# Optimization experiments

Hardware: AMD Instinct MI355X
Metric: run time of the kernel (lower is better)

The kernel has to match this reference:

```python
import jax, jax.numpy as jnp
import numpy as np

D = 512
K = 32
B = 2
L = 2048


def setup_inputs() -> dict:
    key = jax.random.key(0)
    ks = jax.random.split(key, 12)
    s = 1.0 / np.sqrt(D)
    return {
        "x": jax.random.normal(ks[0], (B, L, D), dtype=jnp.float32),
        "W1": jax.random.normal(ks[1], (D, D), dtype=jnp.float32) * s,
        "b1": jnp.zeros((D,), jnp.float32),
        "W2": jax.random.normal(ks[2], (D, K), dtype=jnp.float32) * s,
        "b2": jnp.zeros((K,), jnp.float32),
        "pos_scale": jnp.array([0.5], jnp.float32),
        "content_scale": jnp.array([0.5], jnp.float32),
        "Wv": jax.random.normal(ks[3], (D, D), dtype=jnp.float32) * s,
        "bv": jnp.zeros((D,), jnp.float32),
        "ln_g": jnp.ones((D,), jnp.float32),
        "ln_b": jnp.zeros((D,), jnp.float32),
        "Wo": jax.random.normal(ks[4], (D, D), dtype=jnp.float32) * s,
        "bo": jnp.zeros((D,), jnp.float32),
    }


def reference(x, W1, b1, W2, b2, pos_scale, content_scale, Wv, bv, ln_g, ln_b, Wo, bo):
    Bb, Ll, Dd = x.shape
    Kk = W2.shape[1]
    # fixed positional phases: outer(positions, 1/10000^(k/K))
    freqs = 1.0 / (10000.0 ** (jnp.arange(Kk, dtype=jnp.float32) / Kk))
    pos_phase = jnp.arange(Ll, dtype=jnp.float32)[:, None] * freqs[None, :]  # [L,K]
    # content phase: Linear -> Tanh -> Linear, then tanh * pi
    h = jnp.tanh(x @ W1 + b1)
    content_phase = jnp.tanh(h @ W2 + b2) * jnp.pi  # [B,L,K]
    total_phase = pos_scale * pos_phase[None] + content_scale * content_phase  # [B,L,K]
    value = x @ Wv + bv  # [B,L,D]
    c = jnp.cos(total_phase)
    s = jnp.sin(total_phase)
    # phasor outer-product bind: [B,L,K,D]
    bound_real = c[..., None] * value[:, :, None, :]
    bound_imag = s[..., None] * value[:, :, None, :]
    mem_real = jnp.cumsum(bound_real, axis=1)
    mem_imag = jnp.cumsum(bound_imag, axis=1)
    retrieved = (mem_real * c[..., None] + mem_imag * s[..., None]).sum(axis=2)  # [B,L,D]
    norm = jnp.sqrt(jnp.arange(1, Ll + 1, dtype=jnp.float32) * Kk)[None, :, None]
    retrieved = retrieved / norm
    # to_out: LayerNorm then Linear
    mu = retrieved.mean(axis=-1, keepdims=True)
    var = retrieved.var(axis=-1, keepdims=True)
    ln = (retrieved - mu) / jnp.sqrt(var + 1e-5) * ln_g + ln_b
    return x + ln @ Wo + bo
```

## Files before the change

### kernel.cpp

```cpp
#include <hip/hip_runtime.h>
#include <hip/hip_bf16.h>
#include <math.h>

#define BB   2
#define LL   2048
#define DD   512
#define KK   32
#define BL   (BB*LL)
#define NCH  64

typedef unsigned short ushort_t;
typedef __bf16 bf16x8 __attribute__((ext_vector_type(8)));
typedef float  f32x4  __attribute__((ext_vector_type(4)));
typedef unsigned short ushort8 __attribute__((ext_vector_type(8)));

__device__ __forceinline__ void gl_lds16(const void* g, void* l) {
    __builtin_amdgcn_global_load_lds(
        (const __attribute__((address_space(1))) void*)g,
        (__attribute__((address_space(3))) void*)l, 16, 0, 0);
}
__device__ __forceinline__ ushort_t f2b(float f) {
    __bf16 b = (__bf16)f; return *(ushort_t*)&b;
}
__device__ __forceinline__ float b2f(ushort_t u) {
    unsigned int x = ((unsigned int)u) << 16; return *(float*)&x;
}

__global__ __launch_bounds__(256) void prep(const float* __restrict__ W1,
                                            const float* __restrict__ Wv,
                                            const float* __restrict__ Wo,
                                            const float* __restrict__ W2,
                                            const float* __restrict__ x,
                                            const float* __restrict__ lng,
                                            const float* __restrict__ lnb,
                                            const float* __restrict__ bo,
                                            __hip_bfloat16* __restrict__ Wct,
                                            __hip_bfloat16* __restrict__ Wot,
                                            __hip_bfloat16* __restrict__ W2T,
                                            __hip_bfloat16* __restrict__ xb,
                                            float* __restrict__ Upart,
                                            float* __restrict__ Vpart)
{
    __shared__ float tile[32][33];
    const int bz = blockIdx.z;
    const int tx = threadIdx.x, ty = threadIdx.y;
    const int t = ty * 32 + tx;

    if (bz == 3) {
        const int bid = blockIdx.y * 16 + blockIdx.x;
        const float4* src = (const float4*)x + (size_t)bid * 2048 + t;
        ushort4* dst = (ushort4*)xb + (size_t)bid * 2048 + t;
        #pragma unroll
        for (int i = 0; i < 8; ++i) {
            float4 v = src[i * 256];
            ushort4 o = {f2b(v.x), f2b(v.y), f2b(v.z), f2b(v.w)};
            dst[i * 256] = o;
        }
        return;
    }
    if (bz == 4) {
        if (blockIdx.x != 0) return;
        const int kg = blockIdx.y;
        const int k0 = kg * 32;
        float u0 = 0.f, u1 = 0.f, v0 = 0.f, v1 = 0.f;
        #pragma unroll 4
        for (int k = 0; k < 32; ++k) {
            const float g1 = lng[k0 + k], b1v = lnb[k0 + k];
            const float w0 = Wo[(size_t)(k0 + k) * 512 + t];
            const float w1 = Wo[(size_t)(k0 + k) * 512 + t + 256];
            u0 = fmaf(g1, w0, u0);  u1 = fmaf(g1, w1, u1);
            v0 = fmaf(b1v, w0, v0); v1 = fmaf(b1v, w1, v1);
        }
        if (kg == 0) { v0 += bo[t]; v1 += bo[t + 256]; }
        Upart[kg * 512 + t] = u0;       Upart[kg * 512 + t + 256] = u1;
        Vpart[kg * 512 + t] = v0;       Vpart[kg * 512 + t + 256] = v1;
        return;
    }
    if (bz == 5) {
        if (blockIdx.x != 0) return;
        const int r0 = blockIdx.y * 32;
        #pragma unroll
        for (int i = 0; i < 4; ++i)
            tile[ty + 8 * i][tx] = W2[(size_t)(r0 + ty + 8 * i) * 32 + tx];
        __syncthreads();
        #pragma unroll
        for (int i = 0; i < 4; ++i)
            W2T[(size_t)(ty + 8 * i) * 512 + r0 + tx] =
                __float2bfloat16(tile[tx][ty + 8 * i]);
        return;
    }
    const float* src = bz == 0 ? W1 : (bz == 1 ? Wv : Wo);
    __hip_bfloat16* dst = bz == 0 ? Wct
                        : (bz == 1 ? Wct + 512 * 512 : Wot);
    const int r0 = blockIdx.y * 32, c0 = blockIdx.x * 32;
    #pragma unroll
    for (int i = 0; i < 4; ++i)
        tile[ty + 8 * i][tx] = src[(size_t)(r0 + ty + 8 * i) * 512 + c0 + tx];
    __syncthreads();
    const float sc = (bz == 2) ? lng[r0 + tx] : 1.f;
    #pragma unroll
    for (int i = 0; i < 4; ++i)
        dst[(size_t)(c0 + ty + 8 * i) * 512 + r0 + tx] =
            __float2bfloat16(tile[tx][ty + 8 * i] * sc);
}

template<int BM, int MODE>
__global__ __launch_bounds__(256) void gemm_mfma(
    const ushort_t* __restrict__ A, const ushort_t* __restrict__ Bt,
    const float* __restrict__ bias0, const float* __restrict__ bias1,
    const float* __restrict__ resid,
    __hip_bfloat16* __restrict__ outH, __hip_bfloat16* __restrict__ outV,
    float* __restrict__ outF, const float* __restrict__ stats)
{
    constexpr int WROWS = BM / 2;
    constexpr int MF    = WROWS / 16;
    constexpr int ACH   = BM / 32;
    __shared__ __align__(16) ushort_t As[2][BM * 64];
    __shared__ __align__(16) ushort_t Bs[2][128 * 64];
    __shared__ float muL[BM], rsL[BM], uL[128], vbL[128];

    const int t  = threadIdx.x;
    const int m0 = blockIdx.y * BM, n0 = blockIdx.x * 128;
    const int l  = t & 63, w = t >> 6;
    const int wr = w >> 1, wc = w & 1;
    const int l15 = l & 15, hi = l >> 4;

    if (MODE == 1) {
        if (t < BM) {
            float4 st = *(const float4*)(stats + (size_t)(m0 + t) * 4);
            float s = st.x + st.z, s2 = st.y + st.w;
            float mu = s * (1.f / 512), var = s2 * (1.f / 512) - mu * mu;
            muL[t] = mu;
            rsL[t] = rsqrtf(var + 1e-5f);
        }
        if (t < 128) {
            float u = 0.f, v = 0.f;
            #pragma unroll
            for (int kg = 0; kg < 16; ++kg) {
                u += bias0[kg * 512 + n0 + t];
                v += bias1[kg * 512 + n0 + t];
            }
            uL[t] = u; vbL[t] = v;
        }
    }

    const ushort_t* agp[ACH];
    const ushort_t* bgp[4];
    #pragma unroll
    for (int i = 0; i < ACH; ++i) {
        int row = (t >> 3) + 32 * i, slot = (t & 7) ^ (row & 7);
        agp[i] = A + (size_t)(m0 + row) * 512 + slot * 8;
    }
    #pragma unroll
    for (int i = 0; i < 4; ++i) {
        int row = (t >> 3) + 32 * i, slot = (t & 7) ^ (row & 7);
        bgp[i] = Bt + (size_t)(n0 + row) * 512 + slot * 8;
    }

    int aoff[MF][2], boff[4][2];
    #pragma unroll
    for (int mi = 0; mi < MF; ++mi)
        #pragma unroll
        for (int kh = 0; kh < 2; ++kh) {
            int row = wr * WROWS + mi * 16 + l15;
            aoff[mi][kh] = row * 128 + (((kh * 4 + hi) ^ (row & 7)) * 16);
        }
    #pragma unroll
    for (int nj = 0; nj < 4; ++nj)
        #pragma unroll
        for (int kh = 0; kh < 2; ++kh) {
            int row = wc * 64 + nj * 16 + l15;
            boff[nj][kh] = row * 128 + (((kh * 4 + hi) ^ (row & 7)) * 16);
        }

    f32x4 acc[MF][4];
    #pragma unroll
    for (int mi = 0; mi < MF; ++mi)
        #pragma unroll
        for (int nj = 0; nj < 4; ++nj)
            acc[mi][nj] = f32x4{0.f, 0.f, 0.f, 0.f};

    auto stage = [&](int bs, int k0) {
        #pragma unroll
        for (int i = 0; i < ACH; ++i)
            gl_lds16(agp[i] + k0, (char*)As[bs] + (size_t)(i * 256 + t) * 16);
        #pragma unroll
        for (int i = 0; i < 4; ++i)
            gl_lds16(bgp[i] + k0, (char*)Bs[bs] + (size_t)(i * 256 + t) * 16);
    };

    stage(0, 0);
    for (int ks = 0; ks < 8; ++ks) {
        __syncthreads();
        if (ks < 7) stage((ks + 1) & 1, (ks + 1) * 64);
        const char* as = (const char*)As[ks & 1];
        const char* bsp = (const char*)Bs[ks & 1];
        #pragma unroll
        for (int kh = 0; kh < 2; ++kh) {
            bf16x8 af[MF], bfr[4];
            #pragma unroll
            for (int mi = 0; mi < MF; ++mi)
                af[mi] = *(const bf16x8*)(as + aoff[mi][kh]);
            #pragma unroll
            for (int nj = 0; nj < 4; ++nj)
                bfr[nj] = *(const bf16x8*)(bsp + boff[nj][kh]);
            #pragma unroll
            for (int mi = 0; mi < MF; ++mi)
                #pragma unroll
                for (int nj = 0; nj < 4; ++nj)
                    acc[mi][nj] = __builtin_amdgcn_mfma_f32_16x16x32_bf16(
                        af[mi], bfr[nj], acc[mi][nj], 0, 0, 0);
        }
    }

    #pragma unroll
    for (int nj = 0; nj < 4; ++nj) {
        const int gcol = n0 + wc * 64 + nj * 16 + l15;
        if (MODE == 0) {
            const float bsv = (gcol < 512) ? bias0[gcol] : bias1[gcol - 512];
            #pragma unroll
            for (int mi = 0; mi < MF; ++mi)
                #pragma unroll
                for (int r = 0; r < 4; ++r) {
                    const int grow = m0 + wr * WROWS + mi * 16 + hi * 4 + r;
                    float v = acc[mi][nj][r] + bsv;
                    if (gcol < 512)
                        outH[(size_t)grow * 512 + gcol] = __float2bfloat16(tanhf(v));
                    else
                        outV[(size_t)grow * 512 + (gcol - 512)] = __float2bfloat16(v);
                }
        } else {
            const int lc = wc * 64 + nj * 16 + l15;
            const float uN = uL[lc], vbN = vbL[lc];
            #pragma unroll
            for (int mi = 0; mi < MF; ++mi)
                #pragma unroll
                for (int r = 0; r < 4; ++r) {
                    const int rl = wr * WROWS + mi * 16 + hi * 4 + r;
                    const int grow = m0 + rl;
                    const float rs = rsL[rl], mu = muL[rl];
                    outF[(size_t)grow * 512 + gcol] =
                        resid[(size_t)grow * 512 + gcol]
                        + rs * acc[mi][nj][r] - rs * mu * uN + vbN;
                }
        }
    }
}


__global__ __launch_bounds__(256) void scanA(const __hip_bfloat16* __restrict__ Vb,
                                             const __hip_bfloat16* __restrict__ Hb,
                                             const __hip_bfloat16* __restrict__ W2T,
                                             const float* __restrict__ b2,
                                             const float* __restrict__ ps_p,
                                             const float* __restrict__ cs_p,
                                             ushort_t* __restrict__ CSg,
                                             ushort_t* __restrict__ PPg)
{
    __shared__ __align__(16) ushort_t regA[256 * 64 + 2 * 32 * 40 + 32 * 64];
    __shared__ __align__(16) ushort_t regB[32 * 520];
    ushort_t* Hs  = regA;
    ushort_t* VT  = regA;
    ushort_t* CT  = regA + 256 * 64;
    ushort_t* ST  = regA + 256 * 64 + 32 * 40;
    ushort_t* CSs = regA + 256 * 64 + 2 * 32 * 40;
    ushort_t* W2L = regB;
    ushort_t* PPs = regB;

    const int t = threadIdx.x;
    const int bch = blockIdx.x, dh = blockIdx.y;
    const int b = bch >> 6, ch = bch & 63;
    const size_t vbase = ((size_t)b * LL + ch * 32) * DD + dh * 256;
    const int w = t >> 6, l = t & 63, l15 = l & 15, hi = l >> 4;

    {
        const ushort8* hsrc = (const ushort8*)((const ushort_t*)Hb
                               + ((size_t)b * LL + ch * 32) * DD);
        const ushort8* wsrc = (const ushort8*)((const ushort_t*)W2T);
        #pragma unroll
        for (int i = 0; i < 8; ++i) {
            const int id = i * 256 + t;
            const int row = id >> 6, c8 = id & 63;
            ushort8 hv = hsrc[id];
            ushort8 wv = wsrc[id];
            *(ushort8*)&Hs[row * 520 + c8 * 8] = hv;
            *(ushort8*)&W2L[row * 520 + c8 * 8] = wv;
        }
    }
    __syncthreads();

    f32x4 pacc[2][2];
    #pragma unroll
    for (int mt = 0; mt < 2; ++mt)
        #pragma unroll
        for (int nt = 0; nt < 2; ++nt)
            pacc[mt][nt] = f32x4{0.f,0.f,0.f,0.f};
    for (int ks = 0; ks < 16; ++ks) {
        bf16x8 af[2], bfr[2];
        #pragma unroll
        for (int mt = 0; mt < 2; ++mt)
            af[mt] = *(const bf16x8*)&Hs[(16 * mt + l15) * 520 + ks * 32 + hi * 8];
        #pragma unroll
        for (int nt = 0; nt < 2; ++nt)
            bfr[nt] = *(const bf16x8*)&W2L[(16 * nt + l15) * 520 + ks * 32 + hi * 8];
        #pragma unroll
        for (int mt = 0; mt < 2; ++mt)
            #pragma unroll
            for (int nt = 0; nt < 2; ++nt)
                pacc[mt][nt] = __builtin_amdgcn_mfma_f32_16x16x32_bf16(
                    af[mt], bfr[nt], pacc[mt][nt], 0, 0, 0);
    }
    __syncthreads();

    {
        const float psv = ps_p[0], csv = cs_p[0];
        #pragma unroll
        for (int nt = 0; nt < 2; ++nt) {
            const int kk = l15 + 16 * nt;
            const float freq = exp2f(-(float)kk * (13.287712379549449f / (float)KK));
            const float b2k = b2[kk];
            #pragma unroll
            for (int mt = 0; mt < 2; ++mt) {
                ushort_t cw[4], sw[4];
                #pragma unroll
                for (int r = 0; r < 4; ++r) {
                    const int lloc = 16 * mt + hi * 4 + r;
                    const int lpos = ch * 32 + lloc;
                    const float content = tanhf(pacc[mt][nt][r] + b2k)
                                          * 3.14159265358979323846f * csv;
                    const float total = psv * ((float)lpos * freq) + content;
                    float sv, cv;
                    sincosf(total, &sv, &cv);
                    cw[r] = f2b(cv); sw[r] = f2b(sv);
                    if (dh == 0) {
                        CSs[lloc * 64 + (((kk >> 3) ^ (lloc & 7)) << 3) + (kk & 7)] = cw[r];
                        CSs[lloc * 64 + ((((kk >> 3) + 4) ^ (lloc & 7)) << 3) + (kk & 7)] = sw[r];
                    }
                }
                *(ushort4*)&CT[kk * 40 + 16 * mt + hi * 4] = *(ushort4*)cw;
                *(ushort4*)&ST[kk * 40 + 16 * mt + hi * 4] = *(ushort4*)sw;
            }
        }
    }
    {
        const int lg = t >> 5, dg = t & 31;
        ushort8 r[4];
        #pragma unroll
        for (int i = 0; i < 4; ++i)
            r[i] = *(const ushort8*)((const ushort_t*)Vb + vbase
                                     + (size_t)(lg * 4 + i) * DD + dg * 8);
        const int oct = (lg >> 1) ^ (dg & 7);
        const int sub = (lg & 1) * 4;
        #pragma unroll
        for (int jd = 0; jd < 8; ++jd) {
            ushort4 w4 = {r[0][jd], r[1][jd], r[2][jd], r[3][jd]};
            *(ushort4*)&VT[(dg * 8 + jd) * 64 + oct * 8 + sub] = w4;
        }
    }
    __syncthreads();

    if (dh == 0) {
        ushort_t* cso = CSg + ((size_t)b * NCH + ch) * 2048;
        *(ushort8*)(cso + t * 8) = *(const ushort8*)&CSs[t * 8];
    }

    bf16x8 afc[2], afs[2];
    #pragma unroll
    for (int mt = 0; mt < 2; ++mt) {
        afc[mt] = *(const bf16x8*)&CT[(l15 + 16 * mt) * 40 + hi * 8];
        afs[mt] = *(const bf16x8*)&ST[(l15 + 16 * mt) * 40 + hi * 8];
    }
    f32x4 aPR[2][4], aPI[2][4];
    #pragma unroll
    for (int mt = 0; mt < 2; ++mt)
        #pragma unroll
        for (int nt = 0; nt < 4; ++nt) {
            aPR[mt][nt] = f32x4{0.f,0.f,0.f,0.f};
            aPI[mt][nt] = f32x4{0.f,0.f,0.f,0.f};
        }
    #pragma unroll
    for (int nt = 0; nt < 4; ++nt) {
        const int drow = w * 64 + nt * 16 + l15;
        bf16x8 bv = *(const bf16x8*)&VT[drow * 64 + ((hi ^ ((drow >> 3) & 7)) << 3)];
        #pragma unroll
        for (int mt = 0; mt < 2; ++mt) {
            aPR[mt][nt] = __builtin_amdgcn_mfma_f32_16x16x32_bf16(afc[mt], bv, aPR[mt][nt], 0,0,0);
            aPI[mt][nt] = __builtin_amdgcn_mfma_f32_16x16x32_bf16(afs[mt], bv, aPI[mt][nt], 0,0,0);
        }
    }
    #pragma unroll
    for (int mt = 0; mt < 2; ++mt)
        #pragma unroll
        for (int nt = 0; nt < 4; ++nt) {
            const int dloc = w * 64 + nt * 16 + l15;
            const int kq = 16 * mt + hi * 4;
            const int oR = kq >> 3, oI = 4 + (kq >> 3);
            const int sub = (hi & 1) * 4;
            ushort4 pr4 = {f2b(aPR[mt][nt][0]), f2b(aPR[mt][nt][1]),
                           f2b(aPR[mt][nt][2]), f2b(aPR[mt][nt][3])};
            ushort4 pi4 = {f2b(aPI[mt][nt][0]), f2b(aPI[mt][nt][1]),
                           f2b(aPI[mt][nt][2]), f2b(aPI[mt][nt][3])};
            *(ushort4*)&PPs[dloc * 64 + ((oR ^ (dloc & 7)) * 8) + sub] = pr4;
            *(ushort4*)&PPs[dloc * 64 + ((oI ^ (dloc & 7)) * 8) + sub] = pi4;
        }
    __syncthreads();
    ushort_t* gout = PPg + ((size_t)bch * 512 + dh * 256) * 64;
    #pragma unroll
    for (int i = 0; i < 8; ++i)
        *(ushort8*)(gout + (size_t)(i * 256 + t) * 8) =
            *(const ushort8*)&PPs[(i * 256 + t) * 8];
}

__global__ __launch_bounds__(256) void scan_prefix(ushort_t* __restrict__ PPg)
{
    const int g = blockIdx.x * 256 + threadIdx.x;
    const int b = g >> 15, p = g & 32767;
    float run = 0.f;
    for (int gg = 0; gg < 4; ++gg) {
        ushort_t v[16];
        #pragma unroll
        for (int i = 0; i < 16; ++i)
            v[i] = PPg[(size_t)(b * 64 + gg * 16 + i) * 32768 + p];
        #pragma unroll
        for (int i = 0; i < 16; ++i) {
            ushort_t o = f2b(run);
            run += b2f(v[i]);
            PPg[(size_t)(b * 64 + gg * 16 + i) * 32768 + p] = o;
        }
    }
}

__global__ __launch_bounds__(256) void scanC(__hip_bfloat16* Vb,
                                             const ushort_t* __restrict__ CSg,
                                             const ushort_t* __restrict__ PPg,
                                             float* __restrict__ StatsG)
{
    __shared__ __align__(16) ushort_t VT[256 * 64];
    __shared__ __align__(16) ushort_t PPT[256 * 64];
    __shared__ __align__(16) ushort_t CS[32 * 64];
    __shared__ __align__(16) ushort_t G[32 * 40];
    __shared__ float2 statsL[4][32];

    const int t = threadIdx.x;
    const int bch = blockIdx.x, dh = blockIdx.y;
    const int b = bch >> 6, ch = bch & 63;
    const size_t vbase = ((size_t)b * LL + ch * 32) * DD + dh * 256;

    {
        const ushort_t* ppg = PPg + ((size_t)bch * 512 + dh * 256) * 64;
        #pragma unroll
        for (int i = 0; i < 8; ++i)
            gl_lds16(ppg + (size_t)(i * 256 + t) * 8,
                     (char*)PPT + (size_t)(i * 256 + t) * 16);
        const ushort_t* csg = CSg + ((size_t)b * NCH + ch) * 2048;
        gl_lds16(csg + (size_t)t * 8, (char*)CS + (size_t)t * 16);
    }
    {
        const int lg = t >> 5, dg = t & 31;
        ushort8 r[4];
        #pragma unroll
        for (int i = 0; i < 4; ++i)
            r[i] = *(const ushort8*)((const ushort_t*)Vb + vbase
                                     + (size_t)(lg * 4 + i) * DD + dg * 8);
        const int oct = (lg >> 1) ^ (dg & 7);
        const int sub = (lg & 1) * 4;
        #pragma unroll
        for (int jd = 0; jd < 8; ++jd) {
            ushort4 w4 = {r[0][jd], r[1][jd], r[2][jd], r[3][jd]};
            *(ushort4*)&VT[(dg * 8 + jd) * 64 + oct * 8 + sub] = w4;
        }
    }
    __syncthreads();

    const int w = t >> 6, l = t & 63, l15 = l & 15, hi = l >> 4;

    bf16x8 fc[2], fs[2];
    #pragma unroll
    for (int mt = 0; mt < 2; ++mt) {
        const int row = l15 + 16 * mt;
        fc[mt] = *(const bf16x8*)&CS[row * 64 + ((hi ^ (row & 7)) << 3)];
        fs[mt] = *(const bf16x8*)&CS[row * 64 + (((4 + hi) ^ (row & 7)) << 3)];
    }

    {
        f32x4 gacc[2][2];
        #pragma unroll
        for (int mt = 0; mt < 2; ++mt)
            #pragma unroll
            for (int nt = 0; nt < 2; ++nt) {
                gacc[mt][nt] = f32x4{0.f,0.f,0.f,0.f};
                gacc[mt][nt] = __builtin_amdgcn_mfma_f32_16x16x32_bf16(fc[mt], fc[nt], gacc[mt][nt], 0,0,0);
                gacc[mt][nt] = __builtin_amdgcn_mfma_f32_16x16x32_bf16(fs[mt], fs[nt], gacc[mt][nt], 0,0,0);
            }
        #pragma unroll
        for (int mt = 0; mt < 2; ++mt)
            #pragma unroll
            for (int nt = 0; nt < 2; ++nt)
                #pragma unroll
                for (int r = 0; r < 4; ++r) {
                    const int row = 16 * mt + hi * 4 + r;
                    const int col = 16 * nt + l15;
                    float gv = (col <= row) ? gacc[mt][nt][r] : 0.f;
                    G[row * 40 + col] = f2b(gv);
                }
    }

    bf16x8 ag[2];
    #pragma unroll
    for (int mt = 0; mt < 2; ++mt)
        ag[mt] = *(const bf16x8*)&G[(l15 + 16 * mt) * 40 + hi * 8];

    f32x4 acc[2][4];
    #pragma unroll
    for (int mt = 0; mt < 2; ++mt)
        #pragma unroll
        for (int nt = 0; nt < 4; ++nt)
            acc[mt][nt] = f32x4{0.f,0.f,0.f,0.f};
    #pragma unroll
    for (int nt = 0; nt < 4; ++nt) {
        const int drow = w * 64 + nt * 16 + l15;
        bf16x8 bp0 = *(const bf16x8*)((const char*)PPT + drow * 128 + ((hi ^ (drow & 7)) << 4));
        bf16x8 bp1 = *(const bf16x8*)((const char*)PPT + drow * 128 + (((4 + hi) ^ (drow & 7)) << 4));
        bf16x8 bv  = *(const bf16x8*)&VT[drow * 64 + ((hi ^ ((drow >> 3) & 7)) << 3)];
        #pragma unroll
        for (int mt = 0; mt < 2; ++mt) {
            acc[mt][nt] = __builtin_amdgcn_mfma_f32_16x16x32_bf16(fc[mt], bp0, acc[mt][nt], 0,0,0);
            acc[mt][nt] = __builtin_amdgcn_mfma_f32_16x16x32_bf16(fs[mt], bp1, acc[mt][nt], 0,0,0);
            acc[mt][nt] = __builtin_amdgcn_mfma_f32_16x16x32_bf16(ag[mt], bv,  acc[mt][nt], 0,0,0);
        }
    }

    __syncthreads();
    ushort_t* RTw = VT + w * 2048;

    float sP[2][4] = {}, qP[2][4] = {};
    #pragma unroll
    for (int mt = 0; mt < 2; ++mt)
        #pragma unroll
        for (int nt = 0; nt < 4; ++nt)
            #pragma unroll
            for (int r = 0; r < 4; ++r) {
                const int lrow = 16 * mt + hi * 4 + r;
                const float scale = rsqrtf((float)((ch * 32 + lrow + 1) * KK));
                const float val = acc[mt][nt][r] * scale;
                sP[mt][r] += val;
                qP[mt][r] = fmaf(val, val, qP[mt][r]);
                RTw[lrow * 64 + nt * 16 + l15] = f2b(val);
            }
    #pragma unroll
    for (int c = 0; c < 4; ++c) {
        const int cid = c * 64 + l;
        const int row = cid >> 3, c8 = cid & 7;
        ushort8 v = *(const ushort8*)&RTw[row * 64 + c8 * 8];
        *(ushort8*)((ushort_t*)Vb + ((size_t)b * LL + ch * 32 + row) * DD
                    + dh * 256 + w * 64 + c8 * 8) = v;
    }
    #pragma unroll
    for (int mt = 0; mt < 2; ++mt)
        #pragma unroll
        for (int r = 0; r < 4; ++r) {
            float sv = sP[mt][r], qv = qP[mt][r];
            #pragma unroll
            for (int off = 1; off < 16; off <<= 1) {
                sv += __shfl_xor(sv, off);
                qv += __shfl_xor(qv, off);
            }
            if (l15 == 0)
                statsL[w][16 * mt + hi * 4 + r] = float2{sv, qv};
        }
    __syncthreads();
    if (t < 32) {
        float s = 0.f, q = 0.f;
        #pragma unroll
        for (int w4 = 0; w4 < 4; ++w4) {
            float2 p = statsL[w4][t];
            s += p.x; q += p.y;
        }
        const size_t rowg = (size_t)b * LL + ch * 32 + t;
        *(float2*)&StatsG[(rowg * 2 + dh) * 2] = float2{s, q};
    }
}

extern "C" void kernel_launch(void* const* d_in, const int* in_sizes, int n_in,
                              void* d_out, int out_size, void* d_ws, size_t ws_size,
                              hipStream_t stream)
{
    const float* x   = (const float*)d_in[0];
    const float* W1  = (const float*)d_in[1];
    const float* b1  = (const float*)d_in[2];
    const float* W2  = (const float*)d_in[3];
    const float* b2  = (const float*)d_in[4];
    const float* ps  = (const float*)d_in[5];
    const float* cs  = (const float*)d_in[6];
    const float* Wv  = (const float*)d_in[7];
    const float* bv  = (const float*)d_in[8];
    const float* lng = (const float*)d_in[9];
    const float* lnb = (const float*)d_in[10];
    const float* Wo  = (const float*)d_in[11];
    const float* bo  = (const float*)d_in[12];
    float* out = (float*)d_out;

    char* wsb = (char*)d_ws;
    __hip_bfloat16* Vb  = (__hip_bfloat16*)(wsb);
    ushort_t* PPg = (ushort_t*)(wsb + (4u << 20));
    ushort_t* CSg = (ushort_t*)(wsb + (12u << 20));
    __hip_bfloat16* xb  = (__hip_bfloat16*)(wsb + (13u << 20));
    __hip_bfloat16* Hb  = (__hip_bfloat16*)(wsb + (17u << 20));
    __hip_bfloat16* Wct = (__hip_bfloat16*)(wsb + (21u << 20));
    __hip_bfloat16* Wot = (__hip_bfloat16*)(wsb + (22u << 20));
    float* StatsG = (float*)(wsb + (23u << 20));
    float* Upart  = (float*)(wsb + (23u << 20) + (64u << 10));
    float* Vpart  = (float*)(wsb + (23u << 20) + (96u << 10));
    __hip_bfloat16* W2T = (__hip_bfloat16*)(wsb + (23u << 20) + (128u << 10));

    prep<<<dim3(16, 16, 6), dim3(32, 8), 0, stream>>>(
        W1, Wv, Wo, W2, x, lng, lnb, bo, Wct, Wot, W2T, xb, Upart, Vpart);
    gemm_mfma<64, 0><<<dim3(8, 64), dim3(256), 0, stream>>>(
        (const ushort_t*)xb, (const ushort_t*)Wct, b1, bv, nullptr, Hb, Vb, nullptr, nullptr);
    scanA<<<dim3(BB * NCH, 2), dim3(256), 0, stream>>>(
        Vb, Hb, W2T, b2, ps, cs, CSg, PPg);
    scan_prefix<<<dim3(256), dim3(256), 0, stream>>>(PPg);
    scanC<<<dim3(BB * NCH, 2), dim3(256), 0, stream>>>(Vb, CSg, PPg, StatsG);
    gemm_mfma<32, 1><<<dim3(4, 128), dim3(256), 0, stream>>>(
        (const ushort_t*)Vb, (const ushort_t*)Wot, Upart, Vpart, x, nullptr, nullptr, out, StatsG);
}
```

Measured before the change: 61.23 us.

## Fuse x fp32-to-bf16 conversion into first GEMM A-tile load

Removes the separate x-to-bf16 conversion pass from the prep kernel. The first GEMM now loads fp32 x directly, converts it in registers and stores swizzled bf16 into LDS. The GEMM k-loop also drops LDS double buffering and uses a single buffer with two barriers per step. This saves a 4 MB write and a re-read of xb, but loses load/compute overlap and adds the conversion cost to the GEMM. Each of the 8 N-tiles re-reads fp32 x, which doubles A-operand traffic.

```diff
diff --git a/kernel.cpp b/kernel.cpp
--- a/kernel.cpp
+++ b/kernel.cpp
@@ -30,14 +30,12 @@
                                             const float* __restrict__ Wv,
                                             const float* __restrict__ Wo,
                                             const float* __restrict__ W2,
-                                            const float* __restrict__ x,
                                             const float* __restrict__ lng,
                                             const float* __restrict__ lnb,
                                             const float* __restrict__ bo,
                                             __hip_bfloat16* __restrict__ Wct,
                                             __hip_bfloat16* __restrict__ Wot,
                                             __hip_bfloat16* __restrict__ W2T,
-                                            __hip_bfloat16* __restrict__ xb,
                                             float* __restrict__ Upart,
                                             float* __restrict__ Vpart)
 {
@@ -47,18 +45,6 @@
     const int t = ty * 32 + tx;
 
     if (bz == 3) {
-        const int bid = blockIdx.y * 16 + blockIdx.x;
-        const float4* src = (const float4*)x + (size_t)bid * 2048 + t;
-        ushort4* dst = (ushort4*)xb + (size_t)bid * 2048 + t;
-        #pragma unroll
-        for (int i = 0; i < 8; ++i) {
-            float4 v = src[i * 256];
-            ushort4 o = {f2b(v.x), f2b(v.y), f2b(v.z), f2b(v.w)};
-            dst[i * 256] = o;
-        }
-        return;
-    }
-    if (bz == 4) {
         if (blockIdx.x != 0) return;
         const int kg = blockIdx.y;
         const int k0 = kg * 32;
@@ -76,7 +62,7 @@
         Vpart[kg * 512 + t] = v0;       Vpart[kg * 512 + t + 256] = v1;
         return;
     }
-    if (bz == 5) {
+    if (bz == 4) {
         if (blockIdx.x != 0) return;
         const int r0 = blockIdx.y * 32;
         #pragma unroll
@@ -106,7 +92,8 @@
 
 template<int BM, int MODE>
 __global__ __launch_bounds__(256) void gemm_mfma(
-    const ushort_t* __restrict__ A, const ushort_t* __restrict__ Bt,
+    const ushort_t* __restrict__ A, const float* __restrict__ Af,
+    const ushort_t* __restrict__ Bt,
     const float* __restrict__ bias0, const float* __restrict__ bias1,
     const float* __restrict__ resid,
     __hip_bfloat16* __restrict__ outH, __hip_bfloat16* __restrict__ outV,
@@ -115,8 +102,9 @@
     constexpr int WROWS = BM / 2;
     constexpr int MF    = WROWS / 16;
     constexpr int ACH   = BM / 32;
-    __shared__ __align__(16) ushort_t As[2][BM * 64];
-    __shared__ __align__(16) ushort_t Bs[2][128 * 64];
+    constexpr int ASL   = BM / 32;
+    __shared__ __align__(16) ushort_t As[BM * 64];
+    __shared__ __align__(16) ushort_t Bs[128 * 64];
     __shared__ float muL[BM], rsL[BM], uL[128], vbL[128];
 
     const int t  = threadIdx.x;
@@ -145,12 +133,24 @@
     }
 
     const ushort_t* agp[ACH];
+    const float*    axp[ASL];
+    int             adst[ASL];
+    if (MODE == 0) {
+        #pragma unroll
+        for (int i = 0; i < ASL; ++i) {
+            const int s = i * 256 + t;
+            const int row = s >> 3, c8 = s & 7;
+            axp[i]  = Af + (size_t)(m0 + row) * 512 + c8 * 8;
+            adst[i] = row * 64 + ((c8 ^ (row & 7)) * 8);
+        }
+    } else {
+        #pragma unroll
+        for (int i = 0; i < ACH; ++i) {
+            int row = (t >> 3) + 32 * i, slot = (t & 7) ^ (row & 7);
+            agp[i] = A + (size_t)(m0 + row) * 512 + slot * 8;
+        }
+    }
     const ushort_t* bgp[4];
-    #pragma unroll
-    for (int i = 0; i < ACH; ++i) {
-        int row = (t >> 3) + 32 * i, slot = (t & 7) ^ (row & 7);
-        agp[i] = A + (size_t)(m0 + row) * 512 + slot * 8;
-    }
     #pragma unroll
     for (int i = 0; i < 4; ++i) {
         int row = (t >> 3) + 32 * i, slot = (t & 7) ^ (row & 7);
@@ -180,30 +180,35 @@
         for (int nj = 0; nj < 4; ++nj)
             acc[mi][nj] = f32x4{0.f, 0.f, 0.f, 0.f};
 
-    auto stage = [&](int bs, int k0) {
-        #pragma unroll
-        for (int i = 0; i < ACH; ++i)
-            gl_lds16(agp[i] + k0, (char*)As[bs] + (size_t)(i * 256 + t) * 16);
+    for (int k0 = 0; k0 < 512; k0 += 64) {
+        __syncthreads();
+        if (MODE == 0) {
+            #pragma unroll
+            for (int i = 0; i < ASL; ++i) {
+                float4 v0 = *(const float4*)(axp[i] + k0);
+                float4 v1 = *(const float4*)(axp[i] + k0 + 4);
+                ushort8 o = {f2b(v0.x), f2b(v0.y), f2b(v0.z), f2b(v0.w),
+                             f2b(v1.x), f2b(v1.y), f2b(v1.z), f2b(v1.w)};
+                *(ushort8*)&As[adst[i]] = o;
+            }
+        } else {
+            #pragma unroll
+            for (int i = 0; i < ACH; ++i)
+                gl_lds16(agp[i] + k0, (char*)As + (size_t)(i * 256 + t) * 16);
+        }
         #pragma unroll
         for (int i = 0; i < 4; ++i)
-            gl_lds16(bgp[i] + k0, (char*)Bs[bs] + (size_t)(i * 256 + t) * 16);
-    };
-
-    stage(0, 0);
-    for (int ks = 0; ks < 8; ++ks) {
+            gl_lds16(bgp[i] + k0, (char*)Bs + (size_t)(i * 256 + t) * 16);
         __syncthreads();
-        if (ks < 7) stage((ks + 1) & 1, (ks + 1) * 64);
-        const char* as = (const char*)As[ks & 1];
-        const char* bsp = (const char*)Bs[ks & 1];
         #pragma unroll
         for (int kh = 0; kh < 2; ++kh) {
             bf16x8 af[MF], bfr[4];
             #pragma unroll
             for (int mi = 0; mi < MF; ++mi)
-                af[mi] = *(const bf16x8*)(as + aoff[mi][kh]);
+                af[mi] = *(const bf16x8*)((const char*)As + aoff[mi][kh]);
             #pragma unroll
             for (int nj = 0; nj < 4; ++nj)
-                bfr[nj] = *(const bf16x8*)(bsp + boff[nj][kh]);
+                bfr[nj] = *(const bf16x8*)((const char*)Bs + boff[nj][kh]);
             #pragma unroll
             for (int mi = 0; mi < MF; ++mi)
                 #pragma unroll
@@ -604,23 +609,23 @@
     __hip_bfloat16* Vb  = (__hip_bfloat16*)(wsb);
     ushort_t* PPg = (ushort_t*)(wsb + (4u << 20));
     ushort_t* CSg = (ushort_t*)(wsb + (12u << 20));
-    __hip_bfloat16* xb  = (__hip_bfloat16*)(wsb + (13u << 20));
-    __hip_bfloat16* Hb  = (__hip_bfloat16*)(wsb + (17u << 20));
-    __hip_bfloat16* Wct = (__hip_bfloat16*)(wsb + (21u << 20));
-    __hip_bfloat16* Wot = (__hip_bfloat16*)(wsb + (22u << 20));
-    float* StatsG = (float*)(wsb + (23u << 20));
-    float* Upart  = (float*)(wsb + (23u << 20) + (64u << 10));
-    float* Vpart  = (float*)(wsb + (23u << 20) + (96u << 10));
-    __hip_bfloat16* W2T = (__hip_bfloat16*)(wsb + (23u << 20) + (128u << 10));
-
-    prep<<<dim3(16, 16, 6), dim3(32, 8), 0, stream>>>(
-        W1, Wv, Wo, W2, x, lng, lnb, bo, Wct, Wot, W2T, xb, Upart, Vpart);
+    __hip_bfloat16* Hb  = (__hip_bfloat16*)(wsb + (13u << 20));
+    __hip_bfloat16* Wct = (__hip_bfloat16*)(wsb + (17u << 20));
+    __hip_bfloat16* Wot = (__hip_bfloat16*)(wsb + (18u << 20));
+    float* StatsG = (float*)(wsb + (19u << 20));
+    float* Upart  = (float*)(wsb + (19u << 20) + (64u << 10));
+    float* Vpart  = (float*)(wsb + (19u << 20) + (96u << 10));
+    __hip_bfloat16* W2T = (__hip_bfloat16*)(wsb + (19u << 20) + (128u << 10));
+
+    prep<<<dim3(16, 16, 5), dim3(32, 8), 0, stream>>>(
+        W1, Wv, Wo, W2, lng, lnb, bo, Wct, Wot, W2T, Upart, Vpart);
     gemm_mfma<64, 0><<<dim3(8, 64), dim3(256), 0, stream>>>(
-        (const ushort_t*)xb, (const ushort_t*)Wct, b1, bv, nullptr, Hb, Vb, nullptr, nullptr);
+        nullptr, x, (const ushort_t*)Wct, b1, bv, nullptr, Hb, Vb, nullptr, nullptr);
     scanA<<<dim3(BB * NCH, 2), dim3(256), 0, stream>>>(
         Vb, Hb, W2T, b2, ps, cs, CSg, PPg);
     scan_prefix<<<dim3(256), dim3(256), 0, stream>>>(PPg);
     scanC<<<dim3(BB * NCH, 2), dim3(256), 0, stream>>>(Vb, CSg, PPg, StatsG);
     gemm_mfma<32, 1><<<dim3(4, 128), dim3(256), 0, stream>>>(
-        (const ushort_t*)Vb, (const ushort_t*)Wot, Upart, Vpart, x, nullptr, nullptr, out, StatsG);
-}
+        (const ushort_t*)Vb, nullptr, (const ushort_t*)Wot, Upart, Vpart, x,
+        nullptr, nullptr, out, StatsG);
+}
```

New measurement: 61.21 us. No clear change (-0.0%).
